# Kernel optimization log

Hardware: AMD Instinct MI355X
Metric: run time of the kernel (lower is better)

Reference implementation:

```python
import jax, jax.numpy as jnp
import numpy as np

EPS = 1e-5

def _conv1x1(x, w, b=None):
    # x: (B, Cin, H, W), w: (Cout, Cin) -> (B, Cout, H, W)
    y = jnp.einsum('bchw,oc->bohw', x, w)
    if b is not None:
        y = y + b[None, :, None, None]
    return y

def setup_inputs() -> dict:
    key = jax.random.key(0)
    ks = jax.random.split(key, 14)
    B, C, I = 4, 256, 128
    Ha = Wa = 64
    Hd = Wd = 128
    s = 0.05
    return {
        'detect':  jax.random.normal(ks[0], (B, C, Hd, Wd), jnp.float32),
        'aim':     jax.random.normal(ks[1], (B, C, Ha, Wa), jnp.float32),
        'g_w':     jax.random.normal(ks[2], (I, C), jnp.float32) * s,
        'g_b':     jax.random.normal(ks[3], (I,), jnp.float32) * s,
        'theta_w': jax.random.normal(ks[4], (I, C), jnp.float32) * s,
        'theta_b': jax.random.normal(ks[5], (I,), jnp.float32) * s,
        'phi_w':   jax.random.normal(ks[6], (I, C), jnp.float32) * s,
        'phi_b':   jax.random.normal(ks[7], (I,), jnp.float32) * s,
        'q_w':     jax.random.normal(ks[8], (C, I), jnp.float32) * s,
        'q_b':     jax.random.normal(ks[9], (C,), jnp.float32) * s,
        'bn_gamma': jax.random.normal(ks[10], (C,), jnp.float32),
        'bn_beta':  jax.random.normal(ks[11], (C,), jnp.float32),
        'bn_mean':  jax.random.normal(ks[12], (C,), jnp.float32),
        'bn_var':   jax.random.uniform(ks[13], (C,), jnp.float32) + 0.5,
    }

def reference(detect, aim, g_w, g_b, theta_w, theta_b, phi_w, phi_b,
              q_w, q_b, bn_gamma, bn_beta, bn_mean, bn_var):
    B, C, Hd, Wd = detect.shape
    _, _, Ha, Wa = aim.shape
    Na = Ha * Wa
    Nd = Hd * Wd
    I = g_w.shape[0]

    # 1x1 conv projections, flattened to token sequences
    a_g   = _conv1x1(aim, g_w, g_b).reshape(B, I, Na)        # g(aim)
    th_a  = _conv1x1(aim, theta_w, theta_b).reshape(B, I, Na)
    ph_d  = _conv1x1(detect, phi_w, phi_b).reshape(B, I, Nd)
    # (d_x = g(detect) is dead code in the original forward; omitted)

    # f = theta_x @ phi_x : (B, Na, Nd); permuted -> (B, Nd, Na); N = Na
    f = jnp.einsum('bia,bid->bad', th_a, ph_d)               # (B, Na, Nd)
    inv_n = jnp.float32(1.0 / Na)
    # non_det = (f^T / Na) @ a_x : (B, Nd, I) -> permute -> (B, I, Nd)
    non = jnp.einsum('bad,bia->bid', f * inv_n, a_g)         # (B, I, Nd)
    non = non.reshape(B, I, Hd, Wd)

    # Q: 1x1 conv (I -> C) + BatchNorm (inference mode, running stats)
    y = _conv1x1(non, q_w, q_b)
    inv_std = jax.lax.rsqrt(bn_var + EPS)
    y = (y - bn_mean[None, :, None, None]) * (bn_gamma * inv_std)[None, :, None, None] \
        + bn_beta[None, :, None, None]

    return y + detect
```

## Files before the change

### kernel.cpp

```cpp
#include <hip/hip_runtime.h>

constexpr int BB   = 4;
constexpr int CCH  = 256;
constexpr int IDIM = 128;
constexpr int NAa  = 4096;
constexpr int NDd  = 16384;
constexpr int PAD  = 320;
constexpr float NAinv = 1.0f / 4096.0f;

typedef __bf16 bf16x8 __attribute__((ext_vector_type(8)));
typedef float  f32x4  __attribute__((ext_vector_type(4)));

__device__ inline unsigned short f2bfu(float f) {
    unsigned u = __float_as_uint(f);
    u += 0x7FFFu + ((u >> 16) & 1u);
    return (unsigned short)(u >> 16);
}

__global__ __launch_bounds__(256) void k_conv(const float* __restrict__ aim,
                                              unsigned short* __restrict__ Abf,
                                              float* __restrict__ r) {
    const int row = blockIdx.x;
    const float* src = aim + (long)row * NAa;
    unsigned short* dst = Abf + (long)row * NAa;
    const int t = threadIdx.x;
    float s = 0.f;
    #pragma unroll
    for (int j = 0; j < 4; ++j) {
        const int e = (j * 256 + t) * 4;
        float4 v = *(const float4*)(src + e);
        s += v.x + v.y + v.z + v.w;
        ushort4 o; o.x = f2bfu(v.x); o.y = f2bfu(v.y); o.z = f2bfu(v.z); o.w = f2bfu(v.w);
        *(ushort4*)(dst + e) = o;
    }
    __shared__ float red[256];
    red[t] = s; __syncthreads();
    for (int st = 128; st > 0; st >>= 1) { if (t < st) red[t] += red[t + st]; __syncthreads(); }
    if (t == 0) r[row] = red[0];
}

__global__ __launch_bounds__(256) void k_prep(const float* __restrict__ qw,
                                              const float* __restrict__ gw,
                                              const float* __restrict__ gb,
                                              const float* __restrict__ thw,
                                              const float* __restrict__ thb,
                                              const float* __restrict__ phw,
                                              const float* __restrict__ phb,
                                              float* __restrict__ Phat,
                                              float* __restrict__ Rhat) {
    const int idx = blockIdx.x * 256 + threadIdx.x;
    if (idx < CCH * PAD) {
        const int o = idx / PAD, c = idx - o * PAD;
        float acc = 0.f;
        for (int i = 0; i < IDIM; ++i) {
            const float av = qw[o * IDIM + i];
            const float bv = (c < 256) ? gw[i * CCH + c] : gb[i];
            acc += av * bv;
        }
        if (c > 256) acc = 0.f;
        Phat[idx] = acc;
    } else {
        const int id2 = idx - CCH * PAD;
        const int k = id2 / PAD, c2 = id2 - k * PAD;
        float acc = 0.f;
        for (int i = 0; i < IDIM; ++i) {
            const float av = (k < 256) ? thw[i * CCH + k] : thb[i];
            const float bv = (c2 < 256) ? phw[i * CCH + c2] : phb[i];
            acc += av * bv;
        }
        if (k > 256 || c2 > 256) acc = 0.f;
        Rhat[id2] = acc;
    }
}

__global__ __launch_bounds__(256) void k_S(const unsigned short* __restrict__ Abf,
                                           float* __restrict__ Spart) {
    const int z = blockIdx.z, b = z >> 3, chunk = z & 7;
    const unsigned short* A = Abf + (long)b * CCH * NAa;
    const int t = threadIdx.x, w = t >> 6, lane = t & 63, quad = lane >> 4, l16 = lane & 15;
    const int mb = blockIdx.y * 128 + (w >> 1) * 64;
    const int nb = blockIdx.x * 128 + (w & 1) * 64;
    const int kbase = chunk * 512;
    f32x4 acc[4][4] = {};
    for (int ks = 0; ks < 16; ++ks) {
        const int k = kbase + ks * 32 + quad * 8;
        bf16x8 af[4], bfr[4];
        #pragma unroll
        for (int i = 0; i < 4; ++i) af[i]  = *(const bf16x8*)(A + (long)(mb + i * 16 + l16) * NAa + k);
        #pragma unroll
        for (int j = 0; j < 4; ++j) bfr[j] = *(const bf16x8*)(A + (long)(nb + j * 16 + l16) * NAa + k);
        #pragma unroll
        for (int i = 0; i < 4; ++i)
            #pragma unroll
            for (int j = 0; j < 4; ++j)
                acc[i][j] = __builtin_amdgcn_mfma_f32_16x16x32_bf16(af[i], bfr[j], acc[i][j], 0, 0, 0);
    }
    float* out = Spart + (long)z * CCH * CCH;
    #pragma unroll
    for (int i = 0; i < 4; ++i)
        #pragma unroll
        for (int j = 0; j < 4; ++j)
            #pragma unroll
            for (int reg = 0; reg < 4; ++reg)
                out[(long)(mb + i * 16 + quad * 4 + reg) * CCH + nb + j * 16 + l16] = acc[i][j][reg];
}

__global__ __launch_bounds__(256) void k_red(const float* __restrict__ Spart,
                                             const float* __restrict__ r,
                                             float* __restrict__ Shat) {
    const int b = blockIdx.y;
    const int idx = blockIdx.x * 256 + threadIdx.x;
    const int k = idx / PAD, n = idx - k * PAD;
    float v = 0.f;
    if (k < 256 && n < 256) {
        #pragma unroll
        for (int p = 0; p < 8; ++p)
            v += Spart[(long)(b * 8 + p) * CCH * CCH + k * CCH + n];
    } else if (k == 256 && n < 256) v = r[b * CCH + n];
    else if (n == 256 && k < 256)   v = r[b * CCH + k];
    else if (k == 256 && n == 256)  v = 4096.0f;
    Shat[(long)b * PAD * PAD + idx] = v;
}

__global__ __launch_bounds__(256) void k_T(const float* __restrict__ Phat,
                                           const float* __restrict__ Shat,
                                           float* __restrict__ That) {
    const int b = blockIdx.z;
    const float* Bm = Shat + (long)b * PAD * PAD;
    float* Co = That + (long)b * CCH * PAD;
    const int n0 = blockIdx.x * 64, m0 = blockIdx.y * 64;
    __shared__ float As[16][64], Bs[16][64];
    const int t = threadIdx.x, tm = t >> 4, tn = t & 15;
    float acc[4][4] = {};
    for (int kt = 0; kt < PAD; kt += 16) {
        { const int rr = t >> 2, c4 = (t & 3) << 2;
          float4 v = *(const float4*)(Phat + (long)(m0 + rr) * PAD + kt + c4);
          As[c4][rr] = v.x; As[c4 + 1][rr] = v.y; As[c4 + 2][rr] = v.z; As[c4 + 3][rr] = v.w; }
        { const int rr = t >> 4, c4 = (t & 15) << 2;
          float4 v = *(const float4*)(Bm + (long)(kt + rr) * PAD + n0 + c4);
          Bs[rr][c4] = v.x; Bs[rr][c4 + 1] = v.y; Bs[rr][c4 + 2] = v.z; Bs[rr][c4 + 3] = v.w; }
        __syncthreads();
        #pragma unroll
        for (int kk = 0; kk < 16; ++kk) {
            const float4 a = *(const float4*)&As[kk][tm << 2];
            const float4 bq = *(const float4*)&Bs[kk][tn << 2];
            const float av[4] = {a.x, a.y, a.z, a.w};
            const float bv[4] = {bq.x, bq.y, bq.z, bq.w};
            #pragma unroll
            for (int i = 0; i < 4; ++i)
                #pragma unroll
                for (int j = 0; j < 4; ++j) acc[i][j] += av[i] * bv[j];
        }
        __syncthreads();
    }
    #pragma unroll
    for (int i = 0; i < 4; ++i)
        *(float4*)(Co + (long)(m0 + tm * 4 + i) * PAD + n0 + tn * 4) =
            make_float4(acc[i][0], acc[i][1], acc[i][2], acc[i][3]);
}

__global__ __launch_bounds__(256) void k_w5(const float* __restrict__ That,
                                            const float* __restrict__ Rhat,
                                            const float* __restrict__ qb,
                                            const float* __restrict__ gamma,
                                            const float* __restrict__ beta,
                                            const float* __restrict__ mean,
                                            const float* __restrict__ var,
                                            unsigned short* __restrict__ W5u,
                                            float* __restrict__ b5) {
    const int b = blockIdx.z;
    const float* A = That + (long)b * CCH * PAD;
    const int n0 = blockIdx.x * 64, m0 = blockIdx.y * 64;
    __shared__ float As[16][64], Bs[16][64];
    const int t = threadIdx.x, tm = t >> 4, tn = t & 15;
    float acc[4][4] = {};
    for (int kt = 0; kt < PAD; kt += 16) {
        { const int rr = t >> 2, c4 = (t & 3) << 2;
          float4 v = *(const float4*)(A + (long)(m0 + rr) * PAD + kt + c4);
          As[c4][rr] = v.x; As[c4 + 1][rr] = v.y; As[c4 + 2][rr] = v.z; As[c4 + 3][rr] = v.w; }
        { const int rr = t >> 4, c4 = (t & 15) << 2;
          float4 v = *(const float4*)(Rhat + (long)(kt + rr) * PAD + n0 + c4);
          Bs[rr][c4] = v.x; Bs[rr][c4 + 1] = v.y; Bs[rr][c4 + 2] = v.z; Bs[rr][c4 + 3] = v.w; }
        __syncthreads();
        #pragma unroll
        for (int kk = 0; kk < 16; ++kk) {
            const float4 a = *(const float4*)&As[kk][tm << 2];
            const float4 bq = *(const float4*)&Bs[kk][tn << 2];
            const float av[4] = {a.x, a.y, a.z, a.w};
            const float bv[4] = {bq.x, bq.y, bq.z, bq.w};
            #pragma unroll
            for (int i = 0; i < 4; ++i)
                #pragma unroll
                for (int j = 0; j < 4; ++j) acc[i][j] += av[i] * bv[j];
        }
        __syncthreads();
    }
    #pragma unroll
    for (int i = 0; i < 4; ++i) {
        const int o = m0 + tm * 4 + i;
        const float s = gamma[o] * rsqrtf(var[o] + 1e-5f);
        #pragma unroll
        for (int j = 0; j < 4; ++j) {
            const int c2 = n0 + tn * 4 + j;
            const float val = acc[i][j] * s * NAinv;
            if (c2 < CCH)
                W5u[((long)b * CCH + o) * CCH + c2] = f2bfu(val + (o == c2 ? 1.0f : 0.0f));
            else if (c2 == CCH)
                b5[b * CCH + o] = val + s * (qb[o] - mean[o]) + beta[o];
        }
    }
}

__global__ __launch_bounds__(256) void k_final(const float* __restrict__ detect,
                                               const unsigned short* __restrict__ W5u,
                                               const float* __restrict__ b5,
                                               float* __restrict__ out) {
    const int z = blockIdx.z;
    const int nb = blockIdx.x * 128;
    const int ob = blockIdx.y * 128;
    const float* D = detect + (long)z * CCH * NDd;
    float* O = out + (long)z * CCH * NDd;
    const unsigned short* W = W5u + (long)z * CCH * CCH;
    const int t = threadIdx.x, w = t >> 6, lane = t & 63, quad = lane >> 4, l16 = lane & 15;
    const int mw = (w >> 1) * 64, nw = (w & 1) * 64;
    __shared__ __align__(16) unsigned short lb[128][40];
    f32x4 acc[4][4] = {};
    const int r2 = t >> 4, g = t & 15;
    for (int kt = 0; kt < CCH; kt += 32) {
        #pragma unroll
        for (int e2 = 0; e2 < 2; ++e2) {
            const int nn = g * 8 + e2 * 4;
            float4 x0 = *(const float4*)(D + (long)(kt + 2 * r2) * NDd + nb + nn);
            float4 x1 = *(const float4*)(D + (long)(kt + 2 * r2 + 1) * NDd + nb + nn);
            *(unsigned*)&lb[nn    ][2 * r2] = (unsigned)f2bfu(x0.x) | ((unsigned)f2bfu(x1.x) << 16);
            *(unsigned*)&lb[nn + 1][2 * r2] = (unsigned)f2bfu(x0.y) | ((unsigned)f2bfu(x1.y) << 16);
            *(unsigned*)&lb[nn + 2][2 * r2] = (unsigned)f2bfu(x0.z) | ((unsigned)f2bfu(x1.z) << 16);
            *(unsigned*)&lb[nn + 3][2 * r2] = (unsigned)f2bfu(x0.w) | ((unsigned)f2bfu(x1.w) << 16);
        }
        __syncthreads();
        bf16x8 af[4], bfr[4];
        #pragma unroll
        for (int i = 0; i < 4; ++i)
            af[i] = *(const bf16x8*)(W + (long)(ob + mw + i * 16 + l16) * CCH + kt + quad * 8);
        #pragma unroll
        for (int j = 0; j < 4; ++j)
            bfr[j] = *(const bf16x8*)(&lb[nw + j * 16 + l16][quad * 8]);
        #pragma unroll
        for (int i = 0; i < 4; ++i)
            #pragma unroll
            for (int j = 0; j < 4; ++j)
                acc[i][j] = __builtin_amdgcn_mfma_f32_16x16x32_bf16(af[i], bfr[j], acc[i][j], 0, 0, 0);
        __syncthreads();
    }
    #pragma unroll
    for (int i = 0; i < 4; ++i) {
        float bv[4];
        #pragma unroll
        for (int reg = 0; reg < 4; ++reg)
            bv[reg] = b5[z * CCH + ob + mw + i * 16 + quad * 4 + reg];
        #pragma unroll
        for (int j = 0; j < 4; ++j) {
            const int n = nb + nw + j * 16 + l16;
            #pragma unroll
            for (int reg = 0; reg < 4; ++reg)
                O[(long)(ob + mw + i * 16 + quad * 4 + reg) * NDd + n] = acc[i][j][reg] + bv[reg];
        }
    }
}

extern "C" void kernel_launch(void* const* d_in, const int* in_sizes, int n_in,
                              void* d_out, int out_size, void* d_ws, size_t ws_size,
                              hipStream_t stream) {
    const float* detect = (const float*)d_in[0];
    const float* aim    = (const float*)d_in[1];
    const float* g_w    = (const float*)d_in[2];
    const float* g_b    = (const float*)d_in[3];
    const float* th_w   = (const float*)d_in[4];
    const float* th_b   = (const float*)d_in[5];
    const float* phi_w  = (const float*)d_in[6];
    const float* phi_b  = (const float*)d_in[7];
    const float* q_w    = (const float*)d_in[8];
    const float* q_b    = (const float*)d_in[9];
    const float* gamma  = (const float*)d_in[10];
    const float* beta   = (const float*)d_in[11];
    const float* mean   = (const float*)d_in[12];
    const float* var    = (const float*)d_in[13];
    float* out = (float*)d_out;

    float* ws = (float*)d_ws;
    unsigned short* Abf = (unsigned short*)ws;
    float* r     = ws + 2097152;
    float* Spart = r + 1024;
    float* Shat  = Spart + 2097152;
    float* Phat  = Shat + 409600;
    float* Rhat  = Phat + 81920;
    float* That  = Rhat + 102400;
    unsigned short* W5u = (unsigned short*)(That + 327680);
    float* b5    = That + 327680 + 131072;

    dim3 blk(256);
    k_prep<<<dim3((CCH * PAD + PAD * PAD) / 256), blk, 0, stream>>>(
        q_w, g_w, g_b, th_w, th_b, phi_w, phi_b, Phat, Rhat);
    k_conv<<<dim3(BB * CCH), blk, 0, stream>>>(aim, Abf, r);
    k_S<<<dim3(2, 2, BB * 8), blk, 0, stream>>>(Abf, Spart);
    k_red<<<dim3(PAD * PAD / 256, BB), blk, 0, stream>>>(Spart, r, Shat);
    k_T<<<dim3(5, 4, BB), blk, 0, stream>>>(Phat, Shat, That);
    k_w5<<<dim3(5, 4, BB), blk, 0, stream>>>(That, Rhat, q_b, gamma, beta, mean, var, W5u, b5);
    k_final<<<dim3(NDd / 128, CCH / 128, BB), blk, 0, stream>>>(detect, W5u, b5, out);
}
```

Baseline: 249.3 us.

## Convert small weight GEMMs to bf16 MFMA and double-buffer final GEMM LDS tiles

```diff
diff --git a/kernel.cpp b/kernel.cpp
--- a/kernel.cpp
+++ b/kernel.cpp
@@ -46,44 +46,42 @@
                                               const float* __restrict__ thb,
                                               const float* __restrict__ phw,
                                               const float* __restrict__ phb,
-                                              float* __restrict__ Phat,
-                                              float* __restrict__ Rhat) {
+                                              unsigned short* __restrict__ Ph,
+                                              unsigned short* __restrict__ Rt) {
     const int idx = blockIdx.x * 256 + threadIdx.x;
     if (idx < CCH * PAD) {
         const int o = idx / PAD, c = idx - o * PAD;
         float acc = 0.f;
-        for (int i = 0; i < IDIM; ++i) {
-            const float av = qw[o * IDIM + i];
-            const float bv = (c < 256) ? gw[i * CCH + c] : gb[i];
-            acc += av * bv;
-        }
-        if (c > 256) acc = 0.f;
-        Phat[idx] = acc;
+        if (c <= 256) {
+            for (int i = 0; i < IDIM; ++i)
+                acc += qw[o * IDIM + i] * ((c < 256) ? gw[i * CCH + c] : gb[i]);
+        }
+        Ph[idx] = f2bfu(acc);
     } else {
         const int id2 = idx - CCH * PAD;
-        const int k = id2 / PAD, c2 = id2 - k * PAD;
+        const int c2 = id2 / PAD, k = id2 - c2 * PAD;
         float acc = 0.f;
-        for (int i = 0; i < IDIM; ++i) {
-            const float av = (k < 256) ? thw[i * CCH + k] : thb[i];
-            const float bv = (c2 < 256) ? phw[i * CCH + c2] : phb[i];
-            acc += av * bv;
-        }
-        if (k > 256 || c2 > 256) acc = 0.f;
-        Rhat[id2] = acc;
-    }
-}
-
-__global__ __launch_bounds__(256) void k_S(const unsigned short* __restrict__ Abf,
-                                           float* __restrict__ Spart) {
+        if (k <= 256 && c2 <= 256) {
+            for (int i = 0; i < IDIM; ++i) {
+                const float av = (k < 256) ? thw[i * CCH + k] : thb[i];
+                const float bv = (c2 < 256) ? phw[i * CCH + c2] : phb[i];
+                acc += av * bv;
+            }
+        }
+        Rt[id2] = f2bfu(acc);
+    }
+}
+
+__global__ __launch_bounds__(64) void k_S(const unsigned short* __restrict__ Abf,
+                                          float* __restrict__ Spart) {
     const int z = blockIdx.z, b = z >> 3, chunk = z & 7;
     const unsigned short* A = Abf + (long)b * CCH * NAa;
-    const int t = threadIdx.x, w = t >> 6, lane = t & 63, quad = lane >> 4, l16 = lane & 15;
-    const int mb = blockIdx.y * 128 + (w >> 1) * 64;
-    const int nb = blockIdx.x * 128 + (w & 1) * 64;
-    const int kbase = chunk * 512;
+    const int lane = threadIdx.x, quad = lane >> 4, l16 = lane & 15;
+    const int mb = blockIdx.y * 64, nb = blockIdx.x * 64;
+    const int kb = chunk * 512;
     f32x4 acc[4][4] = {};
     for (int ks = 0; ks < 16; ++ks) {
-        const int k = kbase + ks * 32 + quad * 8;
+        const int k = kb + ks * 32 + quad * 8;
         bf16x8 af[4], bfr[4];
         #pragma unroll
         for (int i = 0; i < 4; ++i) af[i]  = *(const bf16x8*)(A + (long)(mb + i * 16 + l16) * NAa + k);
@@ -95,19 +93,19 @@
             for (int j = 0; j < 4; ++j)
                 acc[i][j] = __builtin_amdgcn_mfma_f32_16x16x32_bf16(af[i], bfr[j], acc[i][j], 0, 0, 0);
     }
-    float* out = Spart + (long)z * CCH * CCH;
+    float* o = Spart + (long)z * CCH * CCH;
     #pragma unroll
     for (int i = 0; i < 4; ++i)
         #pragma unroll
         for (int j = 0; j < 4; ++j)
             #pragma unroll
             for (int reg = 0; reg < 4; ++reg)
-                out[(long)(mb + i * 16 + quad * 4 + reg) * CCH + nb + j * 16 + l16] = acc[i][j][reg];
+                o[(long)(mb + i * 16 + quad * 4 + reg) * CCH + nb + j * 16 + l16] = acc[i][j][reg];
 }
 
 __global__ __launch_bounds__(256) void k_red(const float* __restrict__ Spart,
                                              const float* __restrict__ r,
-                                             float* __restrict__ Shat) {
+                                             unsigned short* __restrict__ Shat) {
     const int b = blockIdx.y;
     const int idx = blockIdx.x * 256 + threadIdx.x;
     const int k = idx / PAD, n = idx - k * PAD;
@@ -119,138 +117,150 @@
     } else if (k == 256 && n < 256) v = r[b * CCH + n];
     else if (n == 256 && k < 256)   v = r[b * CCH + k];
     else if (k == 256 && n == 256)  v = 4096.0f;
-    Shat[(long)b * PAD * PAD + idx] = v;
-}
-
-__global__ __launch_bounds__(256) void k_T(const float* __restrict__ Phat,
-                                           const float* __restrict__ Shat,
-                                           float* __restrict__ That) {
+    Shat[(long)b * PAD * PAD + idx] = f2bfu(v);
+}
+
+__global__ __launch_bounds__(64) void k_t1(const unsigned short* __restrict__ Ph,
+                                           const unsigned short* __restrict__ Sh,
+                                           unsigned short* __restrict__ Th) {
     const int b = blockIdx.z;
-    const float* Bm = Shat + (long)b * PAD * PAD;
-    float* Co = That + (long)b * CCH * PAD;
+    const unsigned short* S = Sh + (long)b * PAD * PAD;
+    unsigned short* T = Th + (long)b * CCH * PAD;
     const int n0 = blockIdx.x * 64, m0 = blockIdx.y * 64;
-    __shared__ float As[16][64], Bs[16][64];
-    const int t = threadIdx.x, tm = t >> 4, tn = t & 15;
-    float acc[4][4] = {};
-    for (int kt = 0; kt < PAD; kt += 16) {
-        { const int rr = t >> 2, c4 = (t & 3) << 2;
-          float4 v = *(const float4*)(Phat + (long)(m0 + rr) * PAD + kt + c4);
-          As[c4][rr] = v.x; As[c4 + 1][rr] = v.y; As[c4 + 2][rr] = v.z; As[c4 + 3][rr] = v.w; }
-        { const int rr = t >> 4, c4 = (t & 15) << 2;
-          float4 v = *(const float4*)(Bm + (long)(kt + rr) * PAD + n0 + c4);
-          Bs[rr][c4] = v.x; Bs[rr][c4 + 1] = v.y; Bs[rr][c4 + 2] = v.z; Bs[rr][c4 + 3] = v.w; }
-        __syncthreads();
-        #pragma unroll
-        for (int kk = 0; kk < 16; ++kk) {
-            const float4 a = *(const float4*)&As[kk][tm << 2];
-            const float4 bq = *(const float4*)&Bs[kk][tn << 2];
-            const float av[4] = {a.x, a.y, a.z, a.w};
-            const float bv[4] = {bq.x, bq.y, bq.z, bq.w};
-            #pragma unroll
-            for (int i = 0; i < 4; ++i)
-                #pragma unroll
-                for (int j = 0; j < 4; ++j) acc[i][j] += av[i] * bv[j];
-        }
-        __syncthreads();
+    const int lane = threadIdx.x, quad = lane >> 4, l16 = lane & 15;
+    f32x4 acc[4][4] = {};
+    for (int kt = 0; kt < PAD; kt += 32) {
+        bf16x8 af[4], bfr[4];
+        #pragma unroll
+        for (int i = 0; i < 4; ++i) af[i]  = *(const bf16x8*)(Ph + (long)(m0 + i * 16 + l16) * PAD + kt + quad * 8);
+        #pragma unroll
+        for (int j = 0; j < 4; ++j) bfr[j] = *(const bf16x8*)(S  + (long)(n0 + j * 16 + l16) * PAD + kt + quad * 8);
+        #pragma unroll
+        for (int i = 0; i < 4; ++i)
+            #pragma unroll
+            for (int j = 0; j < 4; ++j)
+                acc[i][j] = __builtin_amdgcn_mfma_f32_16x16x32_bf16(af[i], bfr[j], acc[i][j], 0, 0, 0);
     }
     #pragma unroll
     for (int i = 0; i < 4; ++i)
-        *(float4*)(Co + (long)(m0 + tm * 4 + i) * PAD + n0 + tn * 4) =
-            make_float4(acc[i][0], acc[i][1], acc[i][2], acc[i][3]);
-}
-
-__global__ __launch_bounds__(256) void k_w5(const float* __restrict__ That,
-                                            const float* __restrict__ Rhat,
-                                            const float* __restrict__ qb,
-                                            const float* __restrict__ gamma,
-                                            const float* __restrict__ beta,
-                                            const float* __restrict__ mean,
-                                            const float* __restrict__ var,
-                                            unsigned short* __restrict__ W5u,
-                                            float* __restrict__ b5) {
+        #pragma unroll
+        for (int j = 0; j < 4; ++j)
+            #pragma unroll
+            for (int reg = 0; reg < 4; ++reg)
+                T[(long)(m0 + i * 16 + quad * 4 + reg) * PAD + n0 + j * 16 + l16] = f2bfu(acc[i][j][reg]);
+}
+
+__global__ __launch_bounds__(64) void k_t2(const unsigned short* __restrict__ Th,
+                                           const unsigned short* __restrict__ Rt,
+                                           const float* __restrict__ qb,
+                                           const float* __restrict__ gamma,
+                                           const float* __restrict__ beta,
+                                           const float* __restrict__ mean,
+                                           const float* __restrict__ var,
+                                           unsigned short* __restrict__ W5u,
+                                           float* __restrict__ b5) {
     const int b = blockIdx.z;
-    const float* A = That + (long)b * CCH * PAD;
+    const unsigned short* A = Th + (long)b * CCH * PAD;
     const int n0 = blockIdx.x * 64, m0 = blockIdx.y * 64;
-    __shared__ float As[16][64], Bs[16][64];
-    const int t = threadIdx.x, tm = t >> 4, tn = t & 15;
-    float acc[4][4] = {};
-    for (int kt = 0; kt < PAD; kt += 16) {
-        { const int rr = t >> 2, c4 = (t & 3) << 2;
-          float4 v = *(const float4*)(A + (long)(m0 + rr) * PAD + kt + c4);
-          As[c4][rr] = v.x; As[c4 + 1][rr] = v.y; As[c4 + 2][rr] = v.z; As[c4 + 3][rr] = v.w; }
-        { const int rr = t >> 4, c4 = (t & 15) << 2;
-          float4 v = *(const float4*)(Rhat + (long)(kt + rr) * PAD + n0 + c4);
-          Bs[rr][c4] = v.x; Bs[rr][c4 + 1] = v.y; Bs[rr][c4 + 2] = v.z; Bs[rr][c4 + 3] = v.w; }
-        __syncthreads();
-        #pragma unroll
-        for (int kk = 0; kk < 16; ++kk) {
-            const float4 a = *(const float4*)&As[kk][tm << 2];
-            const float4 bq = *(const float4*)&Bs[kk][tn << 2];
-            const float av[4] = {a.x, a.y, a.z, a.w};
-            const float bv[4] = {bq.x, bq.y, bq.z, bq.w};
-            #pragma unroll
-            for (int i = 0; i < 4; ++i)
-                #pragma unroll
-                for (int j = 0; j < 4; ++j) acc[i][j] += av[i] * bv[j];
-        }
-        __syncthreads();
+    const int lane = threadIdx.x, quad = lane >> 4, l16 = lane & 15;
+    f32x4 acc[4][4] = {};
+    for (int kt = 0; kt < PAD; kt += 32) {
+        bf16x8 af[4], bfr[4];
+        #pragma unroll
+        for (int i = 0; i < 4; ++i) af[i]  = *(const bf16x8*)(A  + (long)(m0 + i * 16 + l16) * PAD + kt + quad * 8);
+        #pragma unroll
+        for (int j = 0; j < 4; ++j) bfr[j] = *(const bf16x8*)(Rt + (long)(n0 + j * 16 + l16) * PAD + kt + quad * 8);
+        #pragma unroll
+        for (int i = 0; i < 4; ++i)
+            #pragma unroll
+            for (int j = 0; j < 4; ++j)
+                acc[i][j] = __builtin_amdgcn_mfma_f32_16x16x32_bf16(af[i], bfr[j], acc[i][j], 0, 0, 0);
     }
     #pragma unroll
     for (int i = 0; i < 4; ++i) {
-        const int o = m0 + tm * 4 + i;
-        const float s = gamma[o] * rsqrtf(var[o] + 1e-5f);
-        #pragma unroll
-        for (int j = 0; j < 4; ++j) {
-            const int c2 = n0 + tn * 4 + j;
-            const float val = acc[i][j] * s * NAinv;
-            if (c2 < CCH)
-                W5u[((long)b * CCH + o) * CCH + c2] = f2bfu(val + (o == c2 ? 1.0f : 0.0f));
-            else if (c2 == CCH)
-                b5[b * CCH + o] = val + s * (qb[o] - mean[o]) + beta[o];
-        }
-    }
-}
-
-__global__ __launch_bounds__(256) void k_final(const float* __restrict__ detect,
+        #pragma unroll
+        for (int reg = 0; reg < 4; ++reg) {
+            const int o = m0 + i * 16 + quad * 4 + reg;
+            const float s = gamma[o] * rsqrtf(var[o] + 1e-5f);
+            #pragma unroll
+            for (int j = 0; j < 4; ++j) {
+                const int c2 = n0 + j * 16 + l16;
+                const float val = acc[i][j][reg] * s * NAinv;
+                if (c2 < CCH)
+                    W5u[((long)b * CCH + o) * CCH + c2] = f2bfu(val + (o == c2 ? 1.0f : 0.0f));
+                else if (c2 == CCH)
+                    b5[b * CCH + o] = val + s * (qb[o] - mean[o]) + beta[o];
+            }
+        }
+    }
+}
+
+__global__ __launch_bounds__(256) void k_final(const float* __restrict__ D0,
                                                const unsigned short* __restrict__ W5u,
                                                const float* __restrict__ b5,
                                                float* __restrict__ out) {
     const int z = blockIdx.z;
     const int nb = blockIdx.x * 128;
     const int ob = blockIdx.y * 128;
-    const float* D = detect + (long)z * CCH * NDd;
+    const float* D = D0 + (long)z * CCH * NDd;
     float* O = out + (long)z * CCH * NDd;
     const unsigned short* W = W5u + (long)z * CCH * CCH;
-    const int t = threadIdx.x, w = t >> 6, lane = t & 63, quad = lane >> 4, l16 = lane & 15;
-    const int mw = (w >> 1) * 64, nw = (w & 1) * 64;
-    __shared__ __align__(16) unsigned short lb[128][40];
+    const int t = threadIdx.x, wv = t >> 6, lane = t & 63, quad = lane >> 4, l16 = lane & 15;
+    const int mw = (wv >> 1) * 64, nw = (wv & 1) * 64;
+    const int r2 = t >> 4, g = t & 15;
+    __shared__ __align__(16) unsigned short lb[2][128][40];
+    f32x4 x[4];
+
+    auto load_tile = [&](int kt) {
+        const float* base = D + (long)(kt + 2 * r2) * NDd + nb + 8 * g;
+        x[0] = *(const f32x4*)(base);
+        x[1] = *(const f32x4*)(base + NDd);
+        x[2] = *(const f32x4*)(base + 4);
+        x[3] = *(const f32x4*)(base + NDd + 4);
+    };
+    auto write_tile = [&](int buf) {
+        #pragma unroll
+        for (int e2 = 0; e2 < 2; ++e2)
+            #pragma unroll
+            for (int c = 0; c < 4; ++c) {
+                const int n = 8 * g + 4 * e2 + c;
+                const int p = ((n & 7) << 4) + (n >> 3);
+                const unsigned v = (unsigned)f2bfu(x[2 * e2][c]) |
+                                   ((unsigned)f2bfu(x[2 * e2 + 1][c]) << 16);
+                *(unsigned*)&lb[buf][p][2 * r2] = v;
+            }
+    };
+
+    int pj[4];
+    #pragma unroll
+    for (int j = 0; j < 4; ++j) {
+        const int n = nw + j * 16 + l16;
+        pj[j] = ((n & 7) << 4) + (n >> 3);
+    }
+
     f32x4 acc[4][4] = {};
-    const int r2 = t >> 4, g = t & 15;
-    for (int kt = 0; kt < CCH; kt += 32) {
-        #pragma unroll
-        for (int e2 = 0; e2 < 2; ++e2) {
-            const int nn = g * 8 + e2 * 4;
-            float4 x0 = *(const float4*)(D + (long)(kt + 2 * r2) * NDd + nb + nn);
-            float4 x1 = *(const float4*)(D + (long)(kt + 2 * r2 + 1) * NDd + nb + nn);
-            *(unsigned*)&lb[nn    ][2 * r2] = (unsigned)f2bfu(x0.x) | ((unsigned)f2bfu(x1.x) << 16);
-            *(unsigned*)&lb[nn + 1][2 * r2] = (unsigned)f2bfu(x0.y) | ((unsigned)f2bfu(x1.y) << 16);
-            *(unsigned*)&lb[nn + 2][2 * r2] = (unsigned)f2bfu(x0.z) | ((unsigned)f2bfu(x1.z) << 16);
-            *(unsigned*)&lb[nn + 3][2 * r2] = (unsigned)f2bfu(x0.w) | ((unsigned)f2bfu(x1.w) << 16);
-        }
+    load_tile(0);
+    write_tile(0);
+    load_tile(32);
+    for (int it = 0; it < 8; ++it) {
         __syncthreads();
+        const int kt = it * 32;
         bf16x8 af[4], bfr[4];
         #pragma unroll
         for (int i = 0; i < 4; ++i)
             af[i] = *(const bf16x8*)(W + (long)(ob + mw + i * 16 + l16) * CCH + kt + quad * 8);
         #pragma unroll
         for (int j = 0; j < 4; ++j)
-            bfr[j] = *(const bf16x8*)(&lb[nw + j * 16 + l16][quad * 8]);
+            bfr[j] = *(const bf16x8*)&lb[it & 1][pj[j]][quad * 8];
         #pragma unroll
         for (int i = 0; i < 4; ++i)
             #pragma unroll
             for (int j = 0; j < 4; ++j)
                 acc[i][j] = __builtin_amdgcn_mfma_f32_16x16x32_bf16(af[i], bfr[j], acc[i][j], 0, 0, 0);
-        __syncthreads();
+        if (it < 7) {
+            write_tile((it + 1) & 1);
+            if (it < 6) load_tile((it + 2) * 32);
+        }
     }
     #pragma unroll
     for (int i = 0; i < 4; ++i) {
@@ -291,20 +301,20 @@
     unsigned short* Abf = (unsigned short*)ws;
     float* r     = ws + 2097152;
     float* Spart = r + 1024;
-    float* Shat  = Spart + 2097152;
-    float* Phat  = Shat + 409600;
-    float* Rhat  = Phat + 81920;
-    float* That  = Rhat + 102400;
-    unsigned short* W5u = (unsigned short*)(That + 327680);
-    float* b5    = That + 327680 + 131072;
-
-    dim3 blk(256);
-    k_prep<<<dim3((CCH * PAD + PAD * PAD) / 256), blk, 0, stream>>>(
-        q_w, g_w, g_b, th_w, th_b, phi_w, phi_b, Phat, Rhat);
-    k_conv<<<dim3(BB * CCH), blk, 0, stream>>>(aim, Abf, r);
-    k_S<<<dim3(2, 2, BB * 8), blk, 0, stream>>>(Abf, Spart);
-    k_red<<<dim3(PAD * PAD / 256, BB), blk, 0, stream>>>(Spart, r, Shat);
-    k_T<<<dim3(5, 4, BB), blk, 0, stream>>>(Phat, Shat, That);
-    k_w5<<<dim3(5, 4, BB), blk, 0, stream>>>(That, Rhat, q_b, gamma, beta, mean, var, W5u, b5);
-    k_final<<<dim3(NDd / 128, CCH / 128, BB), blk, 0, stream>>>(detect, W5u, b5, out);
-}
+    unsigned short* ub = (unsigned short*)(Spart + 2097152);
+    unsigned short* Shat_u  = ub;
+    unsigned short* Phat_u  = Shat_u + 409600;
+    unsigned short* RhatT_u = Phat_u + 81920;
+    unsigned short* That_u  = RhatT_u + 102400;
+    unsigned short* W5u     = That_u + 327680;
+    float* b5 = (float*)(W5u + 262144);
+
+    k_prep<<<dim3((CCH * PAD + PAD * PAD) / 256), dim3(256), 0, stream>>>(
+        q_w, g_w, g_b, th_w, th_b, phi_w, phi_b, Phat_u, RhatT_u);
+    k_conv<<<dim3(BB * CCH), dim3(256), 0, stream>>>(aim, Abf, r);
+    k_S<<<dim3(4, 4, BB * 8), dim3(64), 0, stream>>>(Abf, Spart);
+    k_red<<<dim3(PAD * PAD / 256, BB), dim3(256), 0, stream>>>(Spart, r, Shat_u);
+    k_t1<<<dim3(5, 4, BB), dim3(64), 0, stream>>>(Phat_u, Shat_u, That_u);
+    k_t2<<<dim3(5, 4, BB), dim3(64), 0, stream>>>(That_u, RhatT_u, q_b, gamma, beta, mean, var, W5u, b5);
+    k_final<<<dim3(NDd / 128, CCH / 128, BB), dim3(256), 0, stream>>>(detect, W5u, b5, out);
+}
```

After: 218.3 us. 1.14x faster.
